# Kernel optimization log

Measured on AMD Instinct MI355X. Metric: run time of the kernel, lower is better.

The kernel has to match this reference:

```python
import jax, jax.numpy as jnp
import numpy as np

B, NW = 1024, 300
N = NW // 3          # 100 tokens (keypoints)
E = 5                # token dim after cat of PE(2): 3 + 2
H, D, L = 4, 64, 3   # heads, d_attention, layers


def setup_inputs() -> dict:
    key = jax.random.key(0)
    ks = jax.random.split(key, 8)
    s = jnp.float32(0.1)
    x = jax.random.normal(ks[0], (B, NW), dtype=jnp.float32)
    Wq = jax.random.normal(ks[1], (L, H, D, E), dtype=jnp.float32) * s  # per-head W_Q (no bias)
    Wk = jax.random.normal(ks[2], (L, H, D, E), dtype=jnp.float32) * s
    Wv = jax.random.normal(ks[3], (L, H, D, E), dtype=jnp.float32) * s
    Wo = jax.random.normal(ks[4], (L, E, H * D), dtype=jnp.float32) * s  # MHA output proj (no bias)
    Wf = jax.random.normal(ks[5], (L, E, E), dtype=jnp.float32) * s      # FFN linear
    bf = jax.random.normal(ks[6], (L, E), dtype=jnp.float32) * s
    g1 = jnp.ones((L, E), dtype=jnp.float32)
    b1 = jnp.zeros((L, E), dtype=jnp.float32)
    g2 = jnp.ones((L, E), dtype=jnp.float32)
    b2 = jnp.zeros((L, E), dtype=jnp.float32)
    return dict(x=x, Wq=Wq, Wk=Wk, Wv=Wv, Wo=Wo, Wf=Wf, bf=bf,
                g1=g1, b1=b1, g2=g2, b2=b2)


def _layer_norm(x, g, b, eps=1e-5):
    mu = jnp.mean(x, axis=-1, keepdims=True)
    var = jnp.mean((x - mu) ** 2, axis=-1, keepdims=True)  # biased, like torch LN
    return (x - mu) / jnp.sqrt(var + eps) * g + b


def reference(x, Wq, Wk, Wv, Wo, Wf, bf, g1, b1, g2, b2):
    kp = x.reshape(B, N, 3)                      # 'b (n d) -> b n d', d=3
    mask = kp[:, :, -1] > 0                      # [B,N] keypoint confidence mask
    # PositionalEncoding(d_model=2, kind='cat'): div_term=[1] -> pe=[sin(pos),cos(pos)]
    pos = jnp.arange(N, dtype=jnp.float32)
    pe = jnp.stack([jnp.sin(pos), jnp.cos(pos)], axis=-1)         # [N,2]
    out = jnp.concatenate([kp, jnp.broadcast_to(pe, (B, N, 2))], axis=-1)  # [B,N,5]
    out = jnp.where(mask[:, :, None], out, jnp.float32(0.0))      # out[~mask]=0

    pair = mask[:, None, None, :] & mask[:, None, :, None]        # [B,1,N,N]
    neg = -jnp.finfo(jnp.float32).max
    scale = jnp.float32(1.0 / np.sqrt(D))
    for l in range(L):
        # per-head projections (heads vectorized over h)
        q = jnp.einsum('bne,hde->bhnd', out, Wq[l])
        k = jnp.einsum('bne,hde->bhnd', out, Wk[l])
        v = jnp.einsum('bne,hde->bhnd', out, Wv[l])
        dots = jnp.einsum('bhid,bhjd->bhij', q, k) * scale        # [B,H,N,N]
        dots = jnp.where(pair, dots, neg)
        attn = jax.nn.softmax(dots, axis=-1)
        o = jnp.einsum('bhij,bhjd->bhid', attn, v)                # [B,H,N,D]
        o = o.transpose(0, 2, 1, 3).reshape(B, N, H * D)          # concat heads
        attn_out = o @ Wo[l].T                                    # [B,N,E]
        ln1 = _layer_norm(attn_out + out, g1[l], b1[l])
        ffn = jax.nn.relu(ln1 @ Wf[l].T + bf[l])
        out = _layer_norm(ffn + ln1, g2[l], b2[l])
    return out
```

## Files before the change

### kernel.cpp

```cpp
#include <hip/hip_runtime.h>
#include <math.h>

#define NTOK 100
#define EDIM 5
#define NH   4
#define NL   3
#define DD   64
#define BLK  256

__device__ __forceinline__ float fexp2(float x){ float r; asm("v_exp_f32 %0, %1" : "=v"(r) : "v"(x)); return r; }
__device__ __forceinline__ float frcp (float x){ float r; asm("v_rcp_f32 %0, %1" : "=v"(r) : "v"(x)); return r; }
__device__ __forceinline__ float frsq (float x){ float r; asm("v_rsq_f32 %0, %1" : "=v"(r) : "v"(x)); return r; }

__global__ void precompute_mp(const float* __restrict__ Wq,
                              const float* __restrict__ Wk,
                              const float* __restrict__ Wv,
                              const float* __restrict__ Wo,
                              float* __restrict__ mp) {
  const int blk = blockIdx.x;
  const int which = blk / 12;
  const int rem = blk % 12;
  const int l = rem / 4, h = rem % 4;
  const int t = threadIdx.x;

  __shared__ float A[320];
  __shared__ float Bsh[320];

  const float* wa = (which ? Wv : Wq) + (l*NH + h)*DD*EDIM;
  for (int r = t; r < 320; r += 64) A[r] = wa[r];
  if (which == 0) {
    const float* wk = Wk + (l*NH + h)*DD*EDIM;
    for (int r = t; r < 320; r += 64) Bsh[r] = wk[r];
  } else {
    for (int r = t; r < 320; r += 64) {
      int f = r >> 6, d = r & 63;
      Bsh[r] = Wo[(l*EDIM + f)*(NH*DD) + h*DD + d];
    }
  }
  __syncthreads();
  if (t < 25) {
    int e = t / 5, f = t % 5;
    float acc = 0.f;
    if (which == 0) {
      #pragma unroll 8
      for (int d = 0; d < DD; ++d) acc += A[d*5+e] * Bsh[d*5+f];
      acc *= 0.125f * 1.44269504088896340736f;
    } else {
      #pragma unroll 8
      for (int d = 0; d < DD; ++d) acc += A[d*5+e] * Bsh[f*64+d];
    }
    mp[which*960 + ((l*NH + h)*EDIM + e)*8 + f] = acc;
  }
}

__global__ __launch_bounds__(BLK, 4) void encoder_kernel(
    const float* __restrict__ x,
    const float* __restrict__ mp,
    const float* __restrict__ Wf,
    const float* __restrict__ bfv,
    const float* __restrict__ g1,
    const float* __restrict__ b1,
    const float* __restrict__ g2,
    const float* __restrict__ b2,
    float* __restrict__ out)
{
  const int b = blockIdx.x, t = threadIdx.x;

  __shared__ float4 s_MP4[480];
  __shared__ float4 s_o4[NTOK+2];
  __shared__ float  s_o1[NTOK+2];
  __shared__ float4 s_w4[2][NH][NTOK+2];
  __shared__ float2 s_w2[2][NH][NTOK+2];
  __shared__ float  s_cf[152];
  __shared__ int    s_cidx[NTOK];
  __shared__ unsigned long long s_bal[2];

  const float* mpf = (const float*)s_MP4;

  for (int r = t; r < 480; r += BLK) s_MP4[r] = ((const float4*)mp)[r];
  for (int r = t; r < 150; r += BLK) {
    float v;
    if      (r <  75) v = Wf[r];
    else if (r <  90) v = bfv[r-75];
    else if (r < 105) v = g1[r-90];
    else if (r < 120) v = b1[r-105];
    else if (r < 135) v = g2[r-120];
    else              v = b2[r-135];
    s_cf[r] = v;
  }

  float k0=0.f, k1=0.f, k2=0.f, msk=0.f;
  if (t < NTOK) {
    k0 = x[b*300 + 3*t];
    k1 = x[b*300 + 3*t + 1];
    k2 = x[b*300 + 3*t + 2];
    msk = (k2 > 0.f) ? 1.f : 0.f;
  }
  unsigned long long bal = __ballot(t < NTOK && msk != 0.f);
  if (t == 0)  s_bal[0] = bal;
  if (t == 64) s_bal[1] = bal;
  __syncthreads();
  const unsigned long long bw0 = s_bal[0], bw1 = s_bal[1];
  const int nm = __builtin_amdgcn_readfirstlane(__popcll(bw0) + __popcll(bw1));
  if (t < NTOK) {
    int lane = t & 63;
    unsigned long long lm = (lane == 0) ? 0ull : ((1ull << lane) - 1ull);
    int pre = (t < 64) ? __popcll(bw0 & lm) : (__popcll(bw0) + __popcll(bw1 & lm));
    if (msk != 0.f) {
      s_o4[pre] = make_float4(k0, k1, k2, __sinf((float)t));
      s_o1[pre] = __cosf((float)t);
      s_cidx[t] = pre;
    } else {
      s_cidx[t] = nm;
    }
  }
  if (t == 0) {
    s_o4[nm]   = make_float4(0.f,0.f,0.f,0.f); s_o1[nm]   = 0.f;
    s_o4[nm+1] = make_float4(0.f,0.f,0.f,0.f); s_o1[nm+1] = 0.f;
  }
  __syncthreads();

  const int hp   = (nm + 2) >> 1;
  const int natt = NH * hp;
  const int nsplit = (2*natt <= BLK) ? 2 : 1;
  const bool task = (t < natt*nsplit);
  int h = 0, i0 = 0, i1 = 0, i1r = 0, jlo = 0, jhi = 0;
  bool rep0 = false, rep1 = false, w1ok = false, corr = false;
  if (task) {
    int g  = t / natt;
    int tt = t - g*natt;
    h = tt / hp; i0 = tt - h*hp; i1 = i0 + hp;
    i1r = (i1 <= nm) ? i1 : nm;
    w1ok = (i1 <= nm);
    rep0 = (i0 == nm); rep1 = (i1 == nm);
    corr = (g == 0);
    int jmid = nm >> 1;
    if (nsplit == 2) { jlo = g ? jmid : 0; jhi = g ? nm : jmid; }
    else             { jlo = 0; jhi = nm; }
  }
  const int wg = task ? (t / natt) : 0;
  const float wext = (float)(NTOK - nm);

  for (int l = 0; l < NL; ++l) {
    if (task) {
      const float* Mh = mpf + ((l*NH + h)*EDIM)*8;
      float4 oA = s_o4[i0];  float oA4 = s_o1[i0];
      float4 oB = s_o4[i1r]; float oB4 = s_o1[i1r];
      float oa[5] = {oA.x, oA.y, oA.z, oA.w, oA4};
      float ob[5] = {oB.x, oB.y, oB.z, oB.w, oB4};
      float a0[5], a1[5];
      #pragma unroll
      for (int f = 0; f < 5; ++f) { a0[f] = 0.f; a1[f] = 0.f; }
      #pragma unroll
      for (int e = 0; e < 5; ++e) {
        float4 mr = *(const float4*)(Mh + e*8); float m4 = Mh[e*8+4];
        float va = oa[e], vb = ob[e];
        a0[0] += va*mr.x; a0[1] += va*mr.y; a0[2] += va*mr.z; a0[3] += va*mr.w; a0[4] += va*m4;
        a1[0] += vb*mr.x; a1[1] += vb*mr.y; a1[2] += vb*mr.z; a1[3] += vb*mr.w; a1[4] += vb*m4;
      }
      if (rep0) { a0[0]=0.f; a0[1]=0.f; a0[2]=0.f; a0[3]=0.f; a0[4]=0.f; }
      if (rep1) { a1[0]=0.f; a1[1]=0.f; a1[2]=0.f; a1[3]=0.f; a1[4]=0.f; }

      float ls0=0.f, ls1=0.f;
      float w00=0.f,w01=0.f,w02=0.f,w03=0.f,w04=0.f;
      float w10=0.f,w11=0.f,w12=0.f,w13=0.f,w14=0.f;
      #pragma unroll 4
      for (int j = jlo; j < jhi; ++j) {
        float4 oj = s_o4[j]; float oe = s_o1[j];
        float s0 = (a0[0]*oj.x + a0[1]*oj.y) + ((a0[2]*oj.z + a0[3]*oj.w) + a0[4]*oe);
        float s1 = (a1[0]*oj.x + a1[1]*oj.y) + ((a1[2]*oj.z + a1[3]*oj.w) + a1[4]*oe);
        float p0 = fexp2(s0);
        float p1 = fexp2(s1);
        ls0 += p0; ls1 += p1;
        w00 += p0*oj.x; w01 += p0*oj.y; w02 += p0*oj.z; w03 += p0*oj.w; w04 += p0*oe;
        w10 += p1*oj.x; w11 += p1*oj.y; w12 += p1*oj.z; w13 += p1*oj.w; w14 += p1*oe;
      }
      if (rep0 && corr) {
        w00 += wext*oa[0]; w01 += wext*oa[1]; w02 += wext*oa[2];
        w03 += wext*oa[3]; w04 += wext*oa[4];
      }
      if (rep1 && corr) {
        w10 += wext*ob[0]; w11 += wext*ob[1]; w12 += wext*ob[2];
        w13 += wext*ob[3]; w14 += wext*ob[4];
      }

      const float* Ph = mpf + 960 + ((l*NH + h)*EDIM)*8;
      float wr0[5] = {w00,w01,w02,w03,w04};
      float wr1[5] = {w10,w11,w12,w13,w14};
      float c00=0.f,c01=0.f,c02=0.f,c03=0.f,c04=0.f;
      float c10=0.f,c11=0.f,c12=0.f,c13=0.f,c14=0.f;
      #pragma unroll
      for (int e = 0; e < 5; ++e) {
        float4 pr = *(const float4*)(Ph + e*8); float p4 = Ph[e*8+4];
        float va = wr0[e], vb = wr1[e];
        c00 += va*pr.x; c01 += va*pr.y; c02 += va*pr.z; c03 += va*pr.w; c04 += va*p4;
        c10 += vb*pr.x; c11 += vb*pr.y; c12 += vb*pr.z; c13 += vb*pr.w; c14 += vb*p4;
      }
      s_w4[wg][h][i0] = make_float4(c00, c01, c02, c03);
      s_w2[wg][h][i0] = make_float2(c04, ls0);
      if (w1ok) {
        s_w4[wg][h][i1] = make_float4(c10, c11, c12, c13);
        s_w2[wg][h][i1] = make_float2(c14, ls1);
      }
    }
    __syncthreads();

    if (t <= nm) {
      int i = t;
      bool rep = (i == nm);
      float4 ov = s_o4[i]; float ov4 = s_o1[i];
      float y[5] = {ov.x, ov.y, ov.z, ov.w, ov4};
      #pragma unroll
      for (int hh = 0; hh < NH; ++hh) {
        float4 wa = s_w4[0][hh][i]; float2 wb = s_w2[0][hh][i];
        float c0 = wa.x, c1 = wa.y, c2 = wa.z, c3 = wa.w, c4 = wb.x;
        float ls = wb.y;
        if (nsplit == 2) {
          float4 wa2 = s_w4[1][hh][i]; float2 wb2 = s_w2[1][hh][i];
          c0 += wa2.x; c1 += wa2.y; c2 += wa2.z; c3 += wa2.w; c4 += wb2.x;
          ls += wb2.y;
        }
        float inv = rep ? 0.01f : frcp(ls);
        y[0] += c0*inv; y[1] += c1*inv; y[2] += c2*inv; y[3] += c3*inv; y[4] += c4*inv;
      }
      float mu = 0.2f*(y[0]+y[1]+y[2]+y[3]+y[4]);
      float var = 0.f;
      #pragma unroll
      for (int e = 0; e < 5; ++e) { float d = y[e]-mu; var += d*d; }
      float iv = frsq(var*0.2f + 1e-5f);
      float l1[5];
      #pragma unroll
      for (int e = 0; e < 5; ++e)
        l1[e] = (y[e]-mu)*iv*s_cf[90+l*5+e] + s_cf[105+l*5+e];
      float r2[5];
      #pragma unroll
      for (int e = 0; e < 5; ++e) {
        float acc = s_cf[75+l*5+e];
        #pragma unroll
        for (int f = 0; f < 5; ++f) acc += l1[f]*s_cf[l*25+e*5+f];
        acc = acc > 0.f ? acc : 0.f;
        r2[e] = acc + l1[e];
      }
      float mu2 = 0.2f*(r2[0]+r2[1]+r2[2]+r2[3]+r2[4]);
      float var2 = 0.f;
      #pragma unroll
      for (int e = 0; e < 5; ++e) { float d = r2[e]-mu2; var2 += d*d; }
      float iv2 = frsq(var2*0.2f + 1e-5f);
      float no0 = (r2[0]-mu2)*iv2*s_cf[120+l*5+0] + s_cf[135+l*5+0];
      float no1 = (r2[1]-mu2)*iv2*s_cf[120+l*5+1] + s_cf[135+l*5+1];
      float no2 = (r2[2]-mu2)*iv2*s_cf[120+l*5+2] + s_cf[135+l*5+2];
      float no3 = (r2[3]-mu2)*iv2*s_cf[120+l*5+3] + s_cf[135+l*5+3];
      float no4 = (r2[4]-mu2)*iv2*s_cf[120+l*5+4] + s_cf[135+l*5+4];
      s_o4[i] = make_float4(no0, no1, no2, no3);
      s_o1[i] = no4;
    }
    __syncthreads();
  }

  for (int r = t; r < NTOK*EDIM; r += BLK) {
    int i = r / EDIM;
    int e = r - i*EDIM;
    int c = s_cidx[i];
    float v = (e < 4) ? ((const float*)&s_o4[c])[e] : s_o1[c];
    out[b*(NTOK*EDIM) + r] = v;
  }
}

extern "C" void kernel_launch(void* const* d_in, const int* in_sizes, int n_in,
                              void* d_out, int out_size, void* d_ws, size_t ws_size,
                              hipStream_t stream) {
  const float* x  = (const float*)d_in[0];
  const float* Wq = (const float*)d_in[1];
  const float* Wk = (const float*)d_in[2];
  const float* Wv = (const float*)d_in[3];
  const float* Wo = (const float*)d_in[4];
  const float* Wf = (const float*)d_in[5];
  const float* bf = (const float*)d_in[6];
  const float* g1 = (const float*)d_in[7];
  const float* b1 = (const float*)d_in[8];
  const float* g2 = (const float*)d_in[9];
  const float* b2 = (const float*)d_in[10];
  float* outp = (float*)d_out;
  float* mp   = (float*)d_ws;

  precompute_mp<<<24, 64, 0, stream>>>(Wq, Wk, Wv, Wo, mp);
  encoder_kernel<<<1024, BLK, 0, stream>>>(x, mp, Wf, bf, g1, b1, g2, b2, outp);
}
```

Before: 116.6 us.

## Map one query row per thread and double block size to 512

Doubles the block size to 512 threads and gives each thread a single query row per head, where before each thread handled two rows. This spreads the attention work over more threads and lowers the serial work and register use per thread, so more latency can be hidden. In exchange each thread reads the shared-memory key list on its own rather than sharing each load across two rows, and fewer blocks may fit per CU because each block is larger and uses more shared memory.

```diff
diff --git a/kernel.cpp b/kernel.cpp
--- a/kernel.cpp
+++ b/kernel.cpp
@@ -6,7 +6,7 @@
 #define NH   4
 #define NL   3
 #define DD   64
-#define BLK  256
+#define BLK  512
 
 __device__ __forceinline__ float fexp2(float x){ float r; asm("v_exp_f32 %0, %1" : "=v"(r) : "v"(x)); return r; }
 __device__ __forceinline__ float frcp (float x){ float r; asm("v_rcp_f32 %0, %1" : "=v"(r) : "v"(x)); return r; }
@@ -120,19 +120,17 @@
   }
   __syncthreads();
 
-  const int hp   = (nm + 2) >> 1;
-  const int natt = NH * hp;
+  const int rowsN = nm + 1;
+  const int natt  = NH * rowsN;
   const int nsplit = (2*natt <= BLK) ? 2 : 1;
   const bool task = (t < natt*nsplit);
-  int h = 0, i0 = 0, i1 = 0, i1r = 0, jlo = 0, jhi = 0;
-  bool rep0 = false, rep1 = false, w1ok = false, corr = false;
+  int h = 0, i0 = 0, jlo = 0, jhi = 0;
+  bool rep0 = false, corr = false;
   if (task) {
     int g  = t / natt;
     int tt = t - g*natt;
-    h = tt / hp; i0 = tt - h*hp; i1 = i0 + hp;
-    i1r = (i1 <= nm) ? i1 : nm;
-    w1ok = (i1 <= nm);
-    rep0 = (i0 == nm); rep1 = (i1 == nm);
+    h = tt / rowsN; i0 = tt - h*rowsN;
+    rep0 = (i0 == nm);
     corr = (g == 0);
     int jmid = nm >> 1;
     if (nsplit == 2) { jlo = g ? jmid : 0; jhi = g ? nm : jmid; }
@@ -145,63 +143,45 @@
     if (task) {
       const float* Mh = mpf + ((l*NH + h)*EDIM)*8;
       float4 oA = s_o4[i0];  float oA4 = s_o1[i0];
-      float4 oB = s_o4[i1r]; float oB4 = s_o1[i1r];
       float oa[5] = {oA.x, oA.y, oA.z, oA.w, oA4};
-      float ob[5] = {oB.x, oB.y, oB.z, oB.w, oB4};
-      float a0[5], a1[5];
-      #pragma unroll
-      for (int f = 0; f < 5; ++f) { a0[f] = 0.f; a1[f] = 0.f; }
+      float a0[5];
+      #pragma unroll
+      for (int f = 0; f < 5; ++f) a0[f] = 0.f;
       #pragma unroll
       for (int e = 0; e < 5; ++e) {
         float4 mr = *(const float4*)(Mh + e*8); float m4 = Mh[e*8+4];
-        float va = oa[e], vb = ob[e];
-        a0[0] += va*mr.x; a0[1] += va*mr.y; a0[2] += va*mr.z; a0[3] += va*mr.w; a0[4] += va*m4;
-        a1[0] += vb*mr.x; a1[1] += vb*mr.y; a1[2] += vb*mr.z; a1[3] += vb*mr.w; a1[4] += vb*m4;
+        float va = oa[e];
+        a0[0] += va*mr.x; a0[1] += va*mr.y; a0[2] += va*mr.z;
+        a0[3] += va*mr.w; a0[4] += va*m4;
       }
       if (rep0) { a0[0]=0.f; a0[1]=0.f; a0[2]=0.f; a0[3]=0.f; a0[4]=0.f; }
-      if (rep1) { a1[0]=0.f; a1[1]=0.f; a1[2]=0.f; a1[3]=0.f; a1[4]=0.f; }
-
-      float ls0=0.f, ls1=0.f;
+
+      float ls0=0.f;
       float w00=0.f,w01=0.f,w02=0.f,w03=0.f,w04=0.f;
-      float w10=0.f,w11=0.f,w12=0.f,w13=0.f,w14=0.f;
-      #pragma unroll 4
+      #pragma unroll 8
       for (int j = jlo; j < jhi; ++j) {
         float4 oj = s_o4[j]; float oe = s_o1[j];
         float s0 = (a0[0]*oj.x + a0[1]*oj.y) + ((a0[2]*oj.z + a0[3]*oj.w) + a0[4]*oe);
-        float s1 = (a1[0]*oj.x + a1[1]*oj.y) + ((a1[2]*oj.z + a1[3]*oj.w) + a1[4]*oe);
         float p0 = fexp2(s0);
-        float p1 = fexp2(s1);
-        ls0 += p0; ls1 += p1;
+        ls0 += p0;
         w00 += p0*oj.x; w01 += p0*oj.y; w02 += p0*oj.z; w03 += p0*oj.w; w04 += p0*oe;
-        w10 += p1*oj.x; w11 += p1*oj.y; w12 += p1*oj.z; w13 += p1*oj.w; w14 += p1*oe;
       }
       if (rep0 && corr) {
         w00 += wext*oa[0]; w01 += wext*oa[1]; w02 += wext*oa[2];
         w03 += wext*oa[3]; w04 += wext*oa[4];
       }
-      if (rep1 && corr) {
-        w10 += wext*ob[0]; w11 += wext*ob[1]; w12 += wext*ob[2];
-        w13 += wext*ob[3]; w14 += wext*ob[4];
-      }
 
       const float* Ph = mpf + 960 + ((l*NH + h)*EDIM)*8;
       float wr0[5] = {w00,w01,w02,w03,w04};
-      float wr1[5] = {w10,w11,w12,w13,w14};
       float c00=0.f,c01=0.f,c02=0.f,c03=0.f,c04=0.f;
-      float c10=0.f,c11=0.f,c12=0.f,c13=0.f,c14=0.f;
       #pragma unroll
       for (int e = 0; e < 5; ++e) {
         float4 pr = *(const float4*)(Ph + e*8); float p4 = Ph[e*8+4];
-        float va = wr0[e], vb = wr1[e];
+        float va = wr0[e];
         c00 += va*pr.x; c01 += va*pr.y; c02 += va*pr.z; c03 += va*pr.w; c04 += va*p4;
-        c10 += vb*pr.x; c11 += vb*pr.y; c12 += vb*pr.z; c13 += vb*pr.w; c14 += vb*p4;
       }
       s_w4[wg][h][i0] = make_float4(c00, c01, c02, c03);
       s_w2[wg][h][i0] = make_float2(c04, ls0);
-      if (w1ok) {
-        s_w4[wg][h][i1] = make_float4(c10, c11, c12, c13);
-        s_w2[wg][h][i1] = make_float2(c14, ls1);
-      }
     }
     __syncthreads();
 
```

Result: no change. 114.5 us (-1.7%).
